# Kernel tuning notes

Hardware: AMD Instinct MI355X
Metric: run time of the kernel (lower is better)

The kernel has to match this reference:

```python
import jax, jax.numpy as jnp
import numpy as np

N_NODES = 8192
D_FEAT = 256


def setup_inputs() -> dict:
    key = jax.random.key(0)
    k1, k2, k3, k4, k5 = jax.random.split(key, 5)
    X = jax.random.normal(k1, (N_NODES, D_FEAT), dtype=jnp.float32)
    # Dense normalized adjacency-like matrix (A_hat); scale by 1/N for stable magnitudes.
    A_hat = jax.random.uniform(k2, (N_NODES, N_NODES), dtype=jnp.float32) / N_NODES
    w_global = jax.random.uniform(k3, (1,), dtype=jnp.float32)
    w_local = jax.random.uniform(k4, (N_NODES,), dtype=jnp.float32)
    W_agg = jax.random.normal(k5, (D_FEAT, D_FEAT), dtype=jnp.float32) / np.sqrt(D_FEAT)
    return {"X": X, "A_hat": A_hat, "w_global": w_global, "w_local": w_local, "W_agg": W_agg}


def reference(X, A_hat, w_global, w_local, W_agg):
    # GCN-style aggregation: f(X, A_hat) = A_hat @ X @ W_agg, then ReLU.
    agg = jax.nn.relu((A_hat @ X) @ W_agg)  # [n, d]
    # xi = sigmoid(w_global) * diag(sigmoid(w_local)); diagonal => elementwise row scale.
    s = (jax.nn.sigmoid(w_global) * jax.nn.sigmoid(w_local))[:, None]  # [n, 1]
    # xi @ agg + (I - xi) @ X  ==  s*agg + X - s*X, fused in one pass.
    return s * agg + X - s * X
```

## Files before the change

### kernel.cpp

```cpp
#include <hip/hip_runtime.h>
#include <hip/hip_bf16.h>


typedef __attribute__((ext_vector_type(4))) float f32x4;
typedef __attribute__((ext_vector_type(8))) __bf16 bf16x8;

#define GLOBAL_AS __attribute__((address_space(1)))
#define LDS_AS __attribute__((address_space(3)))

static __device__ __forceinline__ void gload16(const void* g, void* l) {
  __builtin_amdgcn_global_load_lds((const GLOBAL_AS void*)g, (LDS_AS void*)l, 16, 0, 0);
}
static __device__ __forceinline__ void gload16_stream(const void* g, void* l) {
  __builtin_amdgcn_global_load_lds((const GLOBAL_AS void*)g, (LDS_AS void*)l, 16, 0, 0x12);
}

static __device__ __forceinline__ unsigned short f2bf_bits(float f) {
  __bf16 h = (__bf16)f;
  return __builtin_bit_cast(unsigned short, h);
}

__global__ void prep_kernel(const float* __restrict__ W,
                            const float* __restrict__ wg,
                            const float* __restrict__ wl,
                            unsigned short* __restrict__ WT,
                            float* __restrict__ s) {
  int tid = blockIdx.x * 256 + threadIdx.x;
  int k = tid >> 8, n = tid & 255;
  float w = W[tid];
  int kt = k >> 5, kloc = k & 31;
  WT[kt * 8192 + n * 32 + kloc] = f2bf_bits(w);
  if (tid < 8192) {
    float sg = 1.0f / (1.0f + expf(-wg[0]));
    float sl = 1.0f / (1.0f + expf(-wl[tid]));
    s[tid] = sg * sl;
  }
}

__global__ __launch_bounds__(256, 2) void gemm_xw(
    const float* __restrict__ X,
    const unsigned short* __restrict__ WT,
    unsigned short* __restrict__ XWT2) {
  __shared__ float As[2][32 * 32];
  __shared__ unsigned short Bs[2][128 * 32];

  const int bm = blockIdx.x & 255;
  const int bn = blockIdx.x >> 8;
  const int m0 = bm * 32;
  const int tid = threadIdx.x;
  const int w = tid >> 6;
  const int l = tid & 63;
  const int lr = l & 15;
  const int lq = l >> 4;

  const int pA = w * 1024 + l * 16;
  const int rA = pA >> 7;
  const int qA = (pA >> 4) & 7;
  const int ssA = qA ^ (rA & 7);
  const char* Asrc0 = (const char*)X + (size_t)(m0 + rA) * 1024 + ssA * 16;
  const char* Bsrc0 = (const char*)WT + bn * 8192 + w * 2048 + l * 16;

  f32x4 acc[2][2];
#pragma unroll
  for (int i = 0; i < 2; ++i)
#pragma unroll
    for (int j = 0; j < 2; ++j) acc[i][j] = (f32x4){0.f, 0.f, 0.f, 0.f};

  auto stage = [&](int t, int buf) {
    gload16(Asrc0 + (size_t)t * 128, (char*)&As[buf][0] + w * 1024);
    const char* bs = Bsrc0 + (size_t)t * 16384;
    gload16(bs, (char*)&Bs[buf][0] + w * 2048);
    gload16(bs + 1024, (char*)&Bs[buf][0] + w * 2048 + 1024);
  };

  auto compute = [&](int buf) {
    bf16x8 af[2];
#pragma unroll
    for (int mi = 0; mi < 2; ++mi) {
      int r = mi * 16 + lr;
      const float* ap = &As[buf][r * 32];
      int s0 = (2 * lq) ^ (r & 7);
      int s1 = (2 * lq + 1) ^ (r & 7);
      f32x4 a0 = *(const f32x4*)(ap + s0 * 4);
      f32x4 a1 = *(const f32x4*)(ap + s1 * 4);
      bf16x8 v;
      v[0] = (__bf16)a0.x; v[1] = (__bf16)a0.y; v[2] = (__bf16)a0.z; v[3] = (__bf16)a0.w;
      v[4] = (__bf16)a1.x; v[5] = (__bf16)a1.y; v[6] = (__bf16)a1.z; v[7] = (__bf16)a1.w;
      af[mi] = v;
    }
    bf16x8 bfr[2];
#pragma unroll
    for (int ni = 0; ni < 2; ++ni) {
      int row = w * 32 + ni * 16 + lr;
      bfr[ni] = *(const bf16x8*)(&Bs[buf][row * 32 + lq * 8]);
    }
#pragma unroll
    for (int mi = 0; mi < 2; ++mi)
#pragma unroll
      for (int ni = 0; ni < 2; ++ni)
        acc[mi][ni] = __builtin_amdgcn_mfma_f32_16x16x32_bf16(af[mi], bfr[ni], acc[mi][ni], 0, 0, 0);
  };

  stage(0, 0);
  __syncthreads();
  for (int t = 0; t < 8; ++t) {
    int cur = t & 1;
    if (t + 1 < 8) stage(t + 1, cur ^ 1);
    compute(cur);
    __syncthreads();
  }

#pragma unroll
  for (int mi = 0; mi < 2; ++mi)
#pragma unroll
    for (int ni2 = 0; ni2 < 2; ++ni2) {
      f32x4 z = acc[mi][ni2];
      int n = bn * 128 + w * 32 + ni2 * 16 + lr;
      int k = bm * 32 + mi * 16 + lq * 4;
      int c = k >> 6;
      int kk = (k >> 5) & 1;
      int ni = (n >> 4) & 1;
      int wp = n >> 5;
      int lane2 = (n & 15) + 16 * ((k >> 3) & 3);
      int j0 = k & 7;
      size_t off = (((size_t)c * 8 + wp) * 4 + kk * 2 + ni) * 512 + lane2 * 8 + j0;
      ushort4 u;
      u.x = f2bf_bits(z[0]); u.y = f2bf_bits(z[1]);
      u.z = f2bf_bits(z[2]); u.w = f2bf_bits(z[3]);
      *(ushort4*)(XWT2 + off) = u;
    }
}

template <int NT, bool SPLIT>
__global__ __launch_bounds__(512, 4) void gemm_main(
    const float* __restrict__ A,
    const unsigned short* __restrict__ B2,
    const float* __restrict__ X,
    const float* __restrict__ s,
    float* __restrict__ out,
    float* __restrict__ P) {
  __shared__ float As[4][32 * 64];

  const int bid = blockIdx.x;
  const int m0 = SPLIT ? (bid >> 1) * 32 : bid * 32;
  const int khalf = SPLIT ? (bid & 1) : 0;
  const int tid = threadIdx.x;
  const int w = tid >> 6;
  const int l = tid & 63;
  const int lr = l & 15;
  const int lq = l >> 4;

  const int rA = tid >> 4;
  const int qA = tid & 15;
  const int sqA = qA ^ (rA & 15);
  const char* Asrc =
      (const char*)A + (size_t)(m0 + rA) * 32768 + (size_t)khalf * 16384 + sqA * 16;
  const char* Bbase =
      (const char*)B2 + (size_t)khalf * 64 * 32768 + (size_t)w * 4096 + (size_t)l * 16;

  f32x4 acc[2][2];
#pragma unroll
  for (int i = 0; i < 2; ++i)
#pragma unroll
    for (int j = 0; j < 2; ++j) acc[i][j] = (f32x4){0.f, 0.f, 0.f, 0.f};

  struct BF { bf16x8 a, b, c, d; };
  BF Bf0, Bf1;

  auto stageA = [&](int h, int buf) {
    gload16_stream(Asrc + (size_t)h * 256, (char*)&As[buf][0] + w * 1024);
  };
  auto loadB = [&](int h, BF& f) {
    const char* p = Bbase + (size_t)h * 32768;
    f.a = *(const bf16x8*)(p);
    f.b = *(const bf16x8*)(p + 1024);
    f.c = *(const bf16x8*)(p + 2048);
    f.d = *(const bf16x8*)(p + 3072);
  };

  auto compute = [&](int buf, const BF& f) {
    const char* Ab = (const char*)&As[buf][0];
    bf16x8 af[2][2];
#pragma unroll
    for (int kk = 0; kk < 2; ++kk)
#pragma unroll
      for (int mi = 0; mi < 2; ++mi) {
        int r = mi * 16 + lr;
        int s0 = (kk * 8 + 2 * lq) ^ (r & 15);
        int s1 = ((kk * 8 + 2 * lq) + 1) ^ (r & 15);
        f32x4 a0 = *(const f32x4*)(Ab + r * 256 + s0 * 16);
        f32x4 a1 = *(const f32x4*)(Ab + r * 256 + s1 * 16);
        bf16x8 v;
        v[0] = (__bf16)a0.x; v[1] = (__bf16)a0.y; v[2] = (__bf16)a0.z; v[3] = (__bf16)a0.w;
        v[4] = (__bf16)a1.x; v[5] = (__bf16)a1.y; v[6] = (__bf16)a1.z; v[7] = (__bf16)a1.w;
        af[kk][mi] = v;
      }
    acc[0][0] = __builtin_amdgcn_mfma_f32_16x16x32_bf16(af[0][0], f.a, acc[0][0], 0, 0, 0);
    acc[0][1] = __builtin_amdgcn_mfma_f32_16x16x32_bf16(af[0][0], f.b, acc[0][1], 0, 0, 0);
    acc[1][0] = __builtin_amdgcn_mfma_f32_16x16x32_bf16(af[0][1], f.a, acc[1][0], 0, 0, 0);
    acc[1][1] = __builtin_amdgcn_mfma_f32_16x16x32_bf16(af[0][1], f.b, acc[1][1], 0, 0, 0);
    acc[0][0] = __builtin_amdgcn_mfma_f32_16x16x32_bf16(af[1][0], f.c, acc[0][0], 0, 0, 0);
    acc[0][1] = __builtin_amdgcn_mfma_f32_16x16x32_bf16(af[1][0], f.d, acc[0][1], 0, 0, 0);
    acc[1][0] = __builtin_amdgcn_mfma_f32_16x16x32_bf16(af[1][1], f.c, acc[1][0], 0, 0, 0);
    acc[1][1] = __builtin_amdgcn_mfma_f32_16x16x32_bf16(af[1][1], f.d, acc[1][1], 0, 0, 0);
  };

  stageA(0, 0);
  loadB(0, Bf0);
  stageA(1, 1);
  loadB(1, Bf1);
  stageA(2, 2);
  stageA(3, 3);

  for (int h = 0; h < NT - 4; h += 2) {
    asm volatile("s_waitcnt vmcnt(6)" ::: "memory");
    asm volatile("s_barrier" ::: "memory");
    compute(h & 3, Bf0);
    asm volatile("s_waitcnt lgkmcnt(0)" ::: "memory");
    asm volatile("s_barrier" ::: "memory");
    loadB(h + 2, Bf0);
    stageA(h + 4, h & 3);

    asm volatile("s_waitcnt vmcnt(6)" ::: "memory");
    asm volatile("s_barrier" ::: "memory");
    compute((h + 1) & 3, Bf1);
    asm volatile("s_waitcnt lgkmcnt(0)" ::: "memory");
    asm volatile("s_barrier" ::: "memory");
    loadB(h + 3, Bf1);
    stageA(h + 5, (h + 1) & 3);
  }
  asm volatile("s_waitcnt vmcnt(6)" ::: "memory");
  asm volatile("s_barrier" ::: "memory");
  compute(0, Bf0);
  asm volatile("s_waitcnt lgkmcnt(0)" ::: "memory");
  asm volatile("s_barrier" ::: "memory");
  loadB(NT - 2, Bf0);

  asm volatile("s_waitcnt vmcnt(5)" ::: "memory");
  asm volatile("s_barrier" ::: "memory");
  compute(1, Bf1);
  asm volatile("s_waitcnt lgkmcnt(0)" ::: "memory");
  asm volatile("s_barrier" ::: "memory");
  loadB(NT - 1, Bf1);

  asm volatile("s_waitcnt vmcnt(4)" ::: "memory");
  asm volatile("s_barrier" ::: "memory");
  compute(2, Bf0);
  asm volatile("s_waitcnt lgkmcnt(0)" ::: "memory");
  asm volatile("s_barrier" ::: "memory");

  asm volatile("s_waitcnt vmcnt(0)" ::: "memory");
  asm volatile("s_barrier" ::: "memory");
  compute(3, Bf1);

  if (SPLIT) {
    float* Pb = P + (size_t)khalf * 8192 * 256;
#pragma unroll
    for (int mi = 0; mi < 2; ++mi)
#pragma unroll
      for (int ni = 0; ni < 2; ++ni) {
        f32x4 z = acc[mi][ni];
        int n = w * 32 + ni * 16 + lr;
#pragma unroll
        for (int i = 0; i < 4; ++i) {
          int m = m0 + mi * 16 + lq * 4 + i;
          Pb[m * 256 + n] = z[i];
        }
      }
  } else {
#pragma unroll
    for (int mi = 0; mi < 2; ++mi)
#pragma unroll
      for (int ni = 0; ni < 2; ++ni) {
        f32x4 z = acc[mi][ni];
        int n = w * 32 + ni * 16 + lr;
#pragma unroll
        for (int i = 0; i < 4; ++i) {
          int m = m0 + mi * 16 + lq * 4 + i;
          float x = X[m * 256 + n];
          float sv = s[m];
          out[m * 256 + n] = x + sv * (fmaxf(z[i], 0.f) - x);
        }
      }
  }
}

__global__ __launch_bounds__(256) void finalize_kernel(
    const float* __restrict__ P,
    const float* __restrict__ X,
    const float* __restrict__ s,
    float* __restrict__ out) {
  int i = blockIdx.x * 256 + threadIdx.x;
  int m = i >> 6;
  f32x4 p0 = *(const f32x4*)(P + (size_t)i * 4);
  f32x4 p1 = *(const f32x4*)(P + 2097152 + (size_t)i * 4);
  f32x4 x = *(const f32x4*)(X + (size_t)i * 4);
  float sv = s[m];
  f32x4 o;
#pragma unroll
  for (int j = 0; j < 4; ++j) o[j] = x[j] + sv * (fmaxf(p0[j] + p1[j], 0.f) - x[j]);
  *(f32x4*)(out + (size_t)i * 4) = o;
}

extern "C" void kernel_launch(void* const* d_in, const int* in_sizes, int n_in,
                              void* d_out, int out_size, void* d_ws, size_t ws_size,
                              hipStream_t stream) {
  const float* X = (const float*)d_in[0];
  const float* A = (const float*)d_in[1];
  const float* wg = (const float*)d_in[2];
  const float* wl = (const float*)d_in[3];
  const float* W = (const float*)d_in[4];
  float* out = (float*)d_out;

  unsigned short* XWT2 = (unsigned short*)d_ws;
  unsigned short* WT = (unsigned short*)((char*)d_ws + 4194304);
  float* s = (float*)((char*)d_ws + 4194304 + 131072);
  float* P = (float*)((char*)d_ws + 4194304 + 131072 + 32768);

  prep_kernel<<<256, 256, 0, stream>>>(W, wg, wl, WT, s);
  gemm_xw<<<512, 256, 0, stream>>>(X, WT, XWT2);

  const size_t need = 4194304 + 131072 + 32768 + 2u * 8192 * 256 * 4;
  if (ws_size >= need) {
    gemm_main<64, true><<<512, 512, 0, stream>>>(A, XWT2, X, s, out, P);
    finalize_kernel<<<2048, 256, 0, stream>>>(P, X, s, out);
  } else {
    gemm_main<128, false><<<256, 512, 0, stream>>>(A, XWT2, X, s, out, nullptr);
  }
}
```

Before: 119.7 us.

## Add 8-way split-K GEMM with 128-row tiles and bf16 partials

```diff
diff --git a/kernel.cpp b/kernel.cpp
--- a/kernel.cpp
+++ b/kernel.cpp
@@ -4,6 +4,7 @@
 
 typedef __attribute__((ext_vector_type(4))) float f32x4;
 typedef __attribute__((ext_vector_type(8))) __bf16 bf16x8;
+typedef __attribute__((ext_vector_type(8))) unsigned short u16x8;
 
 #define GLOBAL_AS __attribute__((address_space(1)))
 #define LDS_AS __attribute__((address_space(3)))
@@ -18,6 +19,9 @@
 static __device__ __forceinline__ unsigned short f2bf_bits(float f) {
   __bf16 h = (__bf16)f;
   return __builtin_bit_cast(unsigned short, h);
+}
+static __device__ __forceinline__ float bf2f(unsigned short u) {
+  return __builtin_bit_cast(float, (unsigned)u << 16);
 }
 
 __global__ void prep_kernel(const float* __restrict__ W,
@@ -131,6 +135,124 @@
     }
 }
 
+__global__ __launch_bounds__(512, 4) void gemm_ks8(
+    const float* __restrict__ A,
+    const unsigned short* __restrict__ B2,
+    unsigned short* __restrict__ P) {
+  __shared__ unsigned short Al[2][128 * 40];
+
+  const int bid = blockIdx.x;
+  const int mtile = bid >> 3, kseg = bid & 7;
+  const int m0 = mtile * 128;
+  const int tid = threadIdx.x;
+  const int w = tid >> 6, l = tid & 63;
+  const int lr = l & 15, lq = l >> 4;
+  const int wm = w >> 2, wn = w & 3;
+
+  const int r = tid >> 2, c4 = tid & 3;
+  const float* gA = A + (size_t)(m0 + r) * 8192 + kseg * 1024 + c4 * 8;
+  const int woff = r * 40 + c4 * 8;
+
+  const unsigned short* Bbase = B2 + (size_t)kseg * 262144 + wn * 4096 + l * 8;
+
+  f32x4 acc[4][4];
+#pragma unroll
+  for (int i = 0; i < 4; ++i)
+#pragma unroll
+    for (int j = 0; j < 4; ++j) acc[i][j] = (f32x4){0.f, 0.f, 0.f, 0.f};
+
+  f32x4 sa0, sa1;
+  bf16x8 Bf0, Bf1, Bf2, Bf3;
+
+  auto loadA = [&](int h) {
+    sa0 = *(const f32x4*)(gA + h * 32);
+    sa1 = *(const f32x4*)(gA + h * 32 + 4);
+  };
+  auto writeA = [&](int h) {
+    bf16x8 b;
+    b[0] = (__bf16)sa0.x; b[1] = (__bf16)sa0.y; b[2] = (__bf16)sa0.z; b[3] = (__bf16)sa0.w;
+    b[4] = (__bf16)sa1.x; b[5] = (__bf16)sa1.y; b[6] = (__bf16)sa1.z; b[7] = (__bf16)sa1.w;
+    *(bf16x8*)(&Al[h & 1][woff]) = b;
+  };
+  auto loadB = [&](int h) {
+    const unsigned short* p = Bbase + (h >> 1) * 16384 + (h & 1) * 1024;
+    Bf0 = *(const bf16x8*)(p);
+    Bf1 = *(const bf16x8*)(p + 512);
+    Bf2 = *(const bf16x8*)(p + 2048);
+    Bf3 = *(const bf16x8*)(p + 2560);
+  };
+  auto compute = [&](int h) {
+    const unsigned short* Ab = &Al[h & 1][0];
+#pragma unroll
+    for (int mi = 0; mi < 4; ++mi) {
+      int R = wm * 64 + mi * 16 + lr;
+      bf16x8 af = *(const bf16x8*)(Ab + R * 40 + lq * 8);
+      acc[mi][0] = __builtin_amdgcn_mfma_f32_16x16x32_bf16(af, Bf0, acc[mi][0], 0, 0, 0);
+      acc[mi][1] = __builtin_amdgcn_mfma_f32_16x16x32_bf16(af, Bf1, acc[mi][1], 0, 0, 0);
+      acc[mi][2] = __builtin_amdgcn_mfma_f32_16x16x32_bf16(af, Bf2, acc[mi][2], 0, 0, 0);
+      acc[mi][3] = __builtin_amdgcn_mfma_f32_16x16x32_bf16(af, Bf3, acc[mi][3], 0, 0, 0);
+    }
+  };
+
+  loadA(0);
+  writeA(0);
+  loadB(0);
+  loadA(1);
+  asm volatile("s_waitcnt lgkmcnt(0)" ::: "memory");
+  asm volatile("s_barrier" ::: "memory");
+
+  for (int h = 0; h < 31; ++h) {
+    compute(h);
+    loadB(h + 1);
+    writeA(h + 1);
+    if (h < 30) loadA(h + 2);
+    asm volatile("s_waitcnt lgkmcnt(0)" ::: "memory");
+    asm volatile("s_barrier" ::: "memory");
+  }
+  compute(31);
+
+  unsigned short* Pb = P + (size_t)kseg * (8192 * 256);
+#pragma unroll
+  for (int mi = 0; mi < 4; ++mi)
+#pragma unroll
+    for (int ni = 0; ni < 4; ++ni) {
+      f32x4 z = acc[mi][ni];
+      int n = wn * 64 + ni * 16 + lr;
+#pragma unroll
+      for (int i = 0; i < 4; ++i) {
+        int m = m0 + wm * 64 + mi * 16 + lq * 4 + i;
+        Pb[(size_t)m * 256 + n] = f2bf_bits(z[i]);
+      }
+    }
+}
+
+__global__ __launch_bounds__(256) void finalize8(
+    const unsigned short* __restrict__ P,
+    const float* __restrict__ X,
+    const float* __restrict__ s,
+    float* __restrict__ out) {
+  int i = blockIdx.x * 256 + threadIdx.x;
+  int m = i >> 5;
+  float acc[8] = {0.f, 0.f, 0.f, 0.f, 0.f, 0.f, 0.f, 0.f};
+#pragma unroll
+  for (int ks = 0; ks < 8; ++ks) {
+    u16x8 v = *(const u16x8*)(P + (size_t)ks * 2097152 + (size_t)i * 8);
+#pragma unroll
+    for (int j = 0; j < 8; ++j) acc[j] += bf2f(v[j]);
+  }
+  float sv = s[m];
+  f32x4 x0 = *(const f32x4*)(X + (size_t)i * 8);
+  f32x4 x1 = *(const f32x4*)(X + (size_t)i * 8 + 4);
+  f32x4 o0, o1;
+#pragma unroll
+  for (int j = 0; j < 4; ++j) {
+    o0[j] = x0[j] + sv * (fmaxf(acc[j], 0.f) - x0[j]);
+    o1[j] = x1[j] + sv * (fmaxf(acc[4 + j], 0.f) - x1[j]);
+  }
+  *(f32x4*)(out + (size_t)i * 8) = o0;
+  *(f32x4*)(out + (size_t)i * 8 + 4) = o1;
+}
+
 template <int NT, bool SPLIT>
 __global__ __launch_bounds__(512, 4) void gemm_main(
     const float* __restrict__ A,
@@ -185,11 +307,11 @@
     for (int kk = 0; kk < 2; ++kk)
 #pragma unroll
       for (int mi = 0; mi < 2; ++mi) {
-        int r = mi * 16 + lr;
-        int s0 = (kk * 8 + 2 * lq) ^ (r & 15);
-        int s1 = ((kk * 8 + 2 * lq) + 1) ^ (r & 15);
-        f32x4 a0 = *(const f32x4*)(Ab + r * 256 + s0 * 16);
-        f32x4 a1 = *(const f32x4*)(Ab + r * 256 + s1 * 16);
+        int rr = mi * 16 + lr;
+        int s0 = (kk * 8 + 2 * lq) ^ (rr & 15);
+        int s1 = ((kk * 8 + 2 * lq) + 1) ^ (rr & 15);
+        f32x4 a0 = *(const f32x4*)(Ab + rr * 256 + s0 * 16);
+        f32x4 a1 = *(const f32x4*)(Ab + rr * 256 + s1 * 16);
         bf16x8 v;
         v[0] = (__bf16)a0.x; v[1] = (__bf16)a0.y; v[2] = (__bf16)a0.z; v[3] = (__bf16)a0.w;
         v[4] = (__bf16)a1.x; v[5] = (__bf16)a1.y; v[6] = (__bf16)a1.z; v[7] = (__bf16)a1.w;
@@ -315,15 +437,20 @@
   unsigned short* XWT2 = (unsigned short*)d_ws;
   unsigned short* WT = (unsigned short*)((char*)d_ws + 4194304);
   float* s = (float*)((char*)d_ws + 4194304 + 131072);
-  float* P = (float*)((char*)d_ws + 4194304 + 131072 + 32768);
+  char* Pbase = (char*)d_ws + 4194304 + 131072 + 32768;
 
   prep_kernel<<<256, 256, 0, stream>>>(W, wg, wl, WT, s);
   gemm_xw<<<512, 256, 0, stream>>>(X, WT, XWT2);
 
-  const size_t need = 4194304 + 131072 + 32768 + 2u * 8192 * 256 * 4;
-  if (ws_size >= need) {
-    gemm_main<64, true><<<512, 512, 0, stream>>>(A, XWT2, X, s, out, P);
-    finalize_kernel<<<2048, 256, 0, stream>>>(P, X, s, out);
+  const size_t head = 4194304 + 131072 + 32768;
+  const size_t need8 = head + (size_t)8 * 8192 * 256 * 2;
+  const size_t need2 = head + (size_t)2 * 8192 * 256 * 4;
+  if (ws_size >= need8) {
+    gemm_ks8<<<512, 512, 0, stream>>>(A, XWT2, (unsigned short*)Pbase);
+    finalize8<<<1024, 256, 0, stream>>>((const unsigned short*)Pbase, X, s, out);
+  } else if (ws_size >= need2) {
+    gemm_main<64, true><<<512, 512, 0, stream>>>(A, XWT2, X, s, out, (float*)Pbase);
+    finalize_kernel<<<2048, 256, 0, stream>>>((const float*)Pbase, X, s, out);
   } else {
     gemm_main<128, false><<<256, 512, 0, stream>>>(A, XWT2, X, s, out, nullptr);
   }
```

After: 107.7 us. -10.0%, faster.
